# Optimization experiments

Hardware: AMD Instinct MI355X
Metric: run time of the kernel (lower is better)

## Reference

```python
import jax, jax.numpy as jnp
import numpy as np

B, N, M = 8, 4096, 4096


def setup_inputs() -> dict:
    key = jax.random.key(0)
    k1, k2 = jax.random.split(key)
    tar = jax.random.normal(k1, (B, N, 3), dtype=jnp.float32)
    src = jax.random.normal(k2, (B, M, 3), dtype=jnp.float32)
    return {"tar": tar, "src": src}


def reference(tar, src):
    # diff: [b, n, m, 3]; dist: [b, n, m] Euclidean norm
    diff = tar[:, :, None, :] - src[:, None, :, :]
    dist = jnp.sqrt(jnp.sum(diff * diff, axis=-1))
    # complete: for each target point, min over source points, mean over n -> [b]
    complete = jnp.mean(jnp.min(dist, axis=2), axis=1)
    # accuracy: for each source point, min over target points, mean over m -> [b]
    accuracy = jnp.mean(jnp.min(dist, axis=1), axis=1)
    # reduction='mean' over batch axis
    complete = jnp.mean(complete, axis=-1)
    accuracy = jnp.mean(accuracy, axis=-1)
    chamfer = 0.5 * (complete + accuracy)
    return (accuracy, complete, chamfer)
```

## Files before the change

kernel.cpp:

```cpp
#include <hip/hip_runtime.h>
#include <math.h>

#define B_ 8
#define BIGF 3.4e38f

template <int QPT, int CHUNK>
__global__ __launch_bounds__(256, 4) void minsq_kernel(
    const float* __restrict__ tar, const float* __restrict__ src,
    float* __restrict__ partial, float* __restrict__ outp, int N, int M)
{
    if (blockIdx.x == 0 && blockIdx.y == 0 && blockIdx.z == 0 &&
        threadIdx.x < 3)
        outp[threadIdx.x] = 0.f;

    const int z   = blockIdx.z;
    const int dir = (z >= B_) ? 1 : 0;
    const int b   = dir ? (z - B_) : z;
    const float* __restrict__ qry = dir ? src : tar;
    const float* __restrict__ pts = dir ? tar : src;
    const int K = dir ? M : N;
    const int L = dir ? N : M;

    const int base = blockIdx.y * CHUNK;
    if (base >= L) return;
    const int cnt = min(CHUNK, L - base);

    const size_t SL = (size_t)B_ * (N + M);
    float* __restrict__ out = partial + (size_t)blockIdx.y * SL +
                              (dir ? (size_t)B_ * N : (size_t)0) +
                              (size_t)b * K;

    __shared__ float4 sp[CHUNK];
    const float* __restrict__ p3 = pts + ((size_t)b * L + base) * 3;
    const int t = threadIdx.x;
    for (int i = t; i < cnt; i += 256) {
        float x = p3[3 * i], y = p3[3 * i + 1], zc = p3[3 * i + 2];
        sp[i] = make_float4(x, y, zc, fmaf(x, x, fmaf(y, y, zc * zc)));
    }
    __syncthreads();

    const float* __restrict__ q3 = qry + (size_t)b * K * 3;
    const int qbase = blockIdx.x * (256 * QPT);
    float qx2[QPT], qy2[QPT], qz2[QPT], qw[QPT], mn[QPT];
#pragma unroll
    for (int k = 0; k < QPT; ++k) {
        int qi = qbase + k * 256 + t;
        if (qi < K) {
            float x = q3[3 * qi], y = q3[3 * qi + 1], zc = q3[3 * qi + 2];
            qx2[k] = -2.f * x; qy2[k] = -2.f * y; qz2[k] = -2.f * zc;
            qw[k] = fmaf(x, x, fmaf(y, y, zc * zc));
        } else {
            qx2[k] = 0.f; qy2[k] = 0.f; qz2[k] = 0.f; qw[k] = 0.f;
        }
        mn[k] = BIGF;
    }

    if (cnt == CHUNK) {
#pragma unroll 4
        for (int j = 0; j < CHUNK; j += 2) {
            float4 p0 = sp[j];
            float4 p1 = sp[j + 1];
#pragma unroll
            for (int k = 0; k < QPT; ++k) {
                float d0 = fmaf(qx2[k], p0.x, fmaf(qy2[k], p0.y,
                           fmaf(qz2[k], p0.z, p0.w)));
                float d1 = fmaf(qx2[k], p1.x, fmaf(qy2[k], p1.y,
                           fmaf(qz2[k], p1.z, p1.w)));
                mn[k] = fminf(mn[k], fminf(d0, d1));
            }
        }
    } else {
        int j = 0;
        for (; j + 1 < cnt; j += 2) {
            float4 p0 = sp[j];
            float4 p1 = sp[j + 1];
#pragma unroll
            for (int k = 0; k < QPT; ++k) {
                float d0 = fmaf(qx2[k], p0.x, fmaf(qy2[k], p0.y,
                           fmaf(qz2[k], p0.z, p0.w)));
                float d1 = fmaf(qx2[k], p1.x, fmaf(qy2[k], p1.y,
                           fmaf(qz2[k], p1.z, p1.w)));
                mn[k] = fminf(mn[k], fminf(d0, d1));
            }
        }
        if (j < cnt) {
            float4 p0 = sp[j];
#pragma unroll
            for (int k = 0; k < QPT; ++k) {
                float d0 = fmaf(qx2[k], p0.x, fmaf(qy2[k], p0.y,
                           fmaf(qz2[k], p0.z, p0.w)));
                mn[k] = fminf(mn[k], d0);
            }
        }
    }

#pragma unroll
    for (int k = 0; k < QPT; ++k) {
        int qi = qbase + k * 256 + t;
        if (qi < K) out[qi] = fmaxf(mn[k] + qw[k], 0.f);
    }
}

template <int CHUNK>
__global__ __launch_bounds__(256) void reduce_kernel(
    const float* __restrict__ partial, float* __restrict__ outp,
    int N, int M)
{
    const int nt = B_ * N, ns = B_ * M;
    const size_t SL = (size_t)nt + ns;
    const int slT = (M + CHUNK - 1) / CHUNK;
    const int slS = (N + CHUNK - 1) / CHUNK;
    const int gid = blockIdx.x * 256 + threadIdx.x;
    const int stride = gridDim.x * 256;
    float s_t = 0.f, s_s = 0.f;
    for (int i = gid; i < nt; i += stride) {
        float v = BIGF;
        for (int s = 0; s < slT; ++s)
            v = fminf(v, partial[(size_t)s * SL + i]);
        s_t += sqrtf(v);
    }
    for (int i = gid; i < ns; i += stride) {
        float v = BIGF;
        for (int s = 0; s < slS; ++s)
            v = fminf(v, partial[(size_t)s * SL + nt + i]);
        s_s += sqrtf(v);
    }
#pragma unroll
    for (int off = 32; off > 0; off >>= 1) {
        s_t += __shfl_down(s_t, off);
        s_s += __shfl_down(s_s, off);
    }
    __shared__ float rt[4], rs[4];
    const int wid = threadIdx.x >> 6, lid = threadIdx.x & 63;
    if (lid == 0) { rt[wid] = s_t; rs[wid] = s_s; }
    __syncthreads();
    if (threadIdx.x == 0) {
        float ct = (rt[0] + rt[1] + rt[2] + rt[3]) / (float)nt;
        float ac = (rs[0] + rs[1] + rs[2] + rs[3]) / (float)ns;
        atomicAdd(&outp[0], ac);
        atomicAdd(&outp[1], ct);
        atomicAdd(&outp[2], 0.5f * (ac + ct));
    }
}

extern "C" void kernel_launch(void* const* d_in, const int* in_sizes, int n_in,
                              void* d_out, int out_size, void* d_ws, size_t ws_size,
                              hipStream_t stream) {
    const float* tar = (const float*)d_in[0];
    const float* src = (const float*)d_in[1];
    const int N = in_sizes[0] / (B_ * 3);
    const int M = in_sizes[1] / (B_ * 3);

    float* partial = (float*)d_ws;
    float* outp = (float*)d_out;

    constexpr int QPT = 8, CHUNK = 128;
    const int KL = (N > M) ? N : M;
    const int gx = (KL + 256 * QPT - 1) / (256 * QPT);
    const int gy = (KL + CHUNK - 1) / CHUNK;
    dim3 grid(gx, gy, 2 * B_);
    minsq_kernel<QPT, CHUNK><<<grid, dim3(256), 0, stream>>>(
        tar, src, partial, outp, N, M);

    reduce_kernel<CHUNK><<<dim3(64), dim3(256), 0, stream>>>(
        partial, outp, N, M);
}
```

Measured before the change: 101.1 us.

## Fuse min and reduce via cooperative grid sync with atomicMin buffer

Replaces the per-chunk partial-minimum slices with a single buffer updated by atomicMin on the float bit patterns, which is valid because distances are non-negative. This removes the large partial write and the multi-slice reread in the reduction. The init, min and reduce phases are fused into one cooperative kernel using grid-wide syncs, with a fallback to memsets plus two launches if the cooperative launch fails. The costs are atomic contention on the min buffer, two grid barriers, and a reduction that runs on only 32 blocks.

```diff
diff --git a/kernel.cpp b/kernel.cpp
--- a/kernel.cpp
+++ b/kernel.cpp
@@ -1,34 +1,31 @@
 #include <hip/hip_runtime.h>
+#include <hip/hip_cooperative_groups.h>
 #include <math.h>
+
+namespace cg = cooperative_groups;
 
 #define B_ 8
 #define BIGF 3.4e38f
 
+
 template <int QPT, int CHUNK>
-__global__ __launch_bounds__(256, 4) void minsq_kernel(
+__device__ __forceinline__ void minsq_body(
     const float* __restrict__ tar, const float* __restrict__ src,
-    float* __restrict__ partial, float* __restrict__ outp, int N, int M)
-{
-    if (blockIdx.x == 0 && blockIdx.y == 0 && blockIdx.z == 0 &&
-        threadIdx.x < 3)
-        outp[threadIdx.x] = 0.f;
-
-    const int z   = blockIdx.z;
-    const int dir = (z >= B_) ? 1 : 0;
-    const int b   = dir ? (z - B_) : z;
+    unsigned int* __restrict__ minarr, int N, int M,
+    int bx, int by, int bz)
+{
+    const int dir = (bz >= B_) ? 1 : 0;
+    const int b   = dir ? (bz - B_) : bz;
     const float* __restrict__ qry = dir ? src : tar;
     const float* __restrict__ pts = dir ? tar : src;
     const int K = dir ? M : N;
     const int L = dir ? N : M;
-
-    const int base = blockIdx.y * CHUNK;
+    unsigned int* __restrict__ out =
+        minarr + (dir ? (size_t)B_ * N : (size_t)0) + (size_t)b * K;
+
+    const int base = by * CHUNK;
     if (base >= L) return;
     const int cnt = min(CHUNK, L - base);
-
-    const size_t SL = (size_t)B_ * (N + M);
-    float* __restrict__ out = partial + (size_t)blockIdx.y * SL +
-                              (dir ? (size_t)B_ * N : (size_t)0) +
-                              (size_t)b * K;
 
     __shared__ float4 sp[CHUNK];
     const float* __restrict__ p3 = pts + ((size_t)b * L + base) * 3;
@@ -40,7 +37,7 @@
     __syncthreads();
 
     const float* __restrict__ q3 = qry + (size_t)b * K * 3;
-    const int qbase = blockIdx.x * (256 * QPT);
+    const int qbase = bx * (256 * QPT);
     float qx2[QPT], qy2[QPT], qz2[QPT], qw[QPT], mn[QPT];
 #pragma unroll
     for (int k = 0; k < QPT; ++k) {
@@ -97,33 +94,30 @@
 #pragma unroll
     for (int k = 0; k < QPT; ++k) {
         int qi = qbase + k * 256 + t;
-        if (qi < K) out[qi] = fmaxf(mn[k] + qw[k], 0.f);
-    }
-}
-
-template <int CHUNK>
-__global__ __launch_bounds__(256) void reduce_kernel(
-    const float* __restrict__ partial, float* __restrict__ outp,
-    int N, int M)
+        if (qi < K) {
+            float d2 = fmaxf(mn[k] + qw[k], 0.f);
+            atomicMin(&out[qi], __float_as_uint(d2));
+        }
+    }
+}
+
+__device__ __forceinline__ void reduce_body(
+    unsigned int* __restrict__ minarr, float* __restrict__ outp,
+    int N, int M, int linb, int nblocks)
 {
     const int nt = B_ * N, ns = B_ * M;
-    const size_t SL = (size_t)nt + ns;
-    const int slT = (M + CHUNK - 1) / CHUNK;
-    const int slS = (N + CHUNK - 1) / CHUNK;
-    const int gid = blockIdx.x * 256 + threadIdx.x;
-    const int stride = gridDim.x * 256;
+    const int gid = linb * 256 + threadIdx.x;
+    const int stride = nblocks * 256;
     float s_t = 0.f, s_s = 0.f;
     for (int i = gid; i < nt; i += stride) {
-        float v = BIGF;
-        for (int s = 0; s < slT; ++s)
-            v = fminf(v, partial[(size_t)s * SL + i]);
-        s_t += sqrtf(v);
+        unsigned int u = __hip_atomic_load(&minarr[i], __ATOMIC_RELAXED,
+                                           __HIP_MEMORY_SCOPE_AGENT);
+        s_t += sqrtf(__uint_as_float(u));
     }
     for (int i = gid; i < ns; i += stride) {
-        float v = BIGF;
-        for (int s = 0; s < slS; ++s)
-            v = fminf(v, partial[(size_t)s * SL + nt + i]);
-        s_s += sqrtf(v);
+        unsigned int u = __hip_atomic_load(&minarr[nt + i], __ATOMIC_RELAXED,
+                                           __HIP_MEMORY_SCOPE_AGENT);
+        s_s += sqrtf(__uint_as_float(u));
     }
 #pragma unroll
     for (int off = 32; off > 0; off >>= 1) {
@@ -143,6 +137,44 @@
     }
 }
 
+template <int QPT, int CHUNK>
+__global__ __launch_bounds__(256, 4) void fused_kernel(
+    const float* __restrict__ tar, const float* __restrict__ src,
+    unsigned int* __restrict__ minarr, float* __restrict__ outp, int N, int M)
+{
+    const int linb = ((int)blockIdx.z * gridDim.y + blockIdx.y) * gridDim.x
+                     + blockIdx.x;
+    const int gtid = linb * 256 + (int)threadIdx.x;
+
+    const int tot = B_ * (N + M);
+    if (gtid < tot) minarr[gtid] = 0x7F800000u;
+    if (gtid < 3) outp[gtid] = 0.f;
+
+    cg::this_grid().sync();
+
+    minsq_body<QPT, CHUNK>(tar, src, minarr, N, M,
+                           blockIdx.x, blockIdx.y, blockIdx.z);
+
+    cg::this_grid().sync();
+
+    if (linb < 32) reduce_body(minarr, outp, N, M, linb, 32);
+}
+
+template <int QPT, int CHUNK>
+__global__ __launch_bounds__(256, 4) void minsq_kernel(
+    const float* __restrict__ tar, const float* __restrict__ src,
+    unsigned int* __restrict__ minarr, int N, int M)
+{
+    minsq_body<QPT, CHUNK>(tar, src, minarr, N, M,
+                           blockIdx.x, blockIdx.y, blockIdx.z);
+}
+
+__global__ __launch_bounds__(256) void reduce_kernel(
+    unsigned int* __restrict__ minarr, float* __restrict__ outp, int N, int M)
+{
+    reduce_body(minarr, outp, N, M, blockIdx.x, gridDim.x);
+}
+
 extern "C" void kernel_launch(void* const* d_in, const int* in_sizes, int n_in,
                               void* d_out, int out_size, void* d_ws, size_t ws_size,
                               hipStream_t stream) {
@@ -151,7 +183,7 @@
     const int N = in_sizes[0] / (B_ * 3);
     const int M = in_sizes[1] / (B_ * 3);
 
-    float* partial = (float*)d_ws;
+    unsigned int* minarr = (unsigned int*)d_ws;
     float* outp = (float*)d_out;
 
     constexpr int QPT = 8, CHUNK = 128;
@@ -159,9 +191,20 @@
     const int gx = (KL + 256 * QPT - 1) / (256 * QPT);
     const int gy = (KL + CHUNK - 1) / CHUNK;
     dim3 grid(gx, gy, 2 * B_);
-    minsq_kernel<QPT, CHUNK><<<grid, dim3(256), 0, stream>>>(
-        tar, src, partial, outp, N, M);
-
-    reduce_kernel<CHUNK><<<dim3(64), dim3(256), 0, stream>>>(
-        partial, outp, N, M);
-}
+    dim3 block(256);
+
+    void* args[] = {(void*)&tar, (void*)&src, (void*)&minarr,
+                    (void*)&outp, (void*)&N, (void*)&M};
+    hipError_t err = hipLaunchCooperativeKernel(
+        (const void*)&fused_kernel<QPT, CHUNK>, grid, block, args, 0, stream);
+
+    if (err != hipSuccess) {
+        (void)hipGetLastError();
+        hipMemsetAsync(minarr, 0xFF,
+                       (size_t)B_ * (N + M) * sizeof(unsigned int), stream);
+        hipMemsetAsync(outp, 0, 3 * sizeof(float), stream);
+        minsq_kernel<QPT, CHUNK><<<grid, block, 0, stream>>>(
+            tar, src, minarr, N, M);
+        reduce_kernel<<<dim3(32), block, 0, stream>>>(minarr, outp, N, M);
+    }
+}
```

Result: slower. 217.6 us (+115.3%).
